# Kernel optimization log

Hardware: AMD Instinct MI355X
Metric: run time of the kernel (lower is better)

## Reference

```python
import jax, jax.numpy as jnp
import numpy as np

N_IN, C, T, E, N_OUT, F = 50000, 64, 8, 800000, 50000, 64


def setup_inputs() -> dict:
    key = jax.random.key(0)
    k0, k1, k2, k3, k4 = jax.random.split(key, 5)
    node_features = jax.random.normal(k0, (N_IN, C), dtype=jnp.float32)
    edge_features = jax.random.normal(k1, (T, E), dtype=jnp.float32)
    idx_out = jax.random.randint(k2, (E,), 0, N_OUT)
    idx_in = jax.random.randint(k3, (E,), 0, N_IN)
    indices = jnp.stack([idx_out, idx_in], axis=1).astype(jnp.int64)  # [E, 2]
    # glorot-ish scale for kernel [T, C, F]
    scale = np.sqrt(2.0 / (C + F)).astype(np.float32)
    kernel = jax.random.normal(k4, (T, C, F), dtype=jnp.float32) * scale
    bias = jnp.zeros((F,), dtype=jnp.float32)
    return {
        "node_features": node_features,
        "edge_features": edge_features,
        "indices": indices,
        "kernel": kernel,
        "bias": bias,
        "out_size": N_OUT,
    }


def reference(node_features, edge_features, indices, kernel, bias, out_size):
    # sparse_conv (combine='unstack'):
    #   out[i] = sum_t ( segment_sum_{e: out(e)=i} ef[t,e] * x[in(e)] ) @ kernel[t] + bias
    gathered = node_features[indices[:, 1]]          # [E, C] irregular gather
    seg_ids = indices[:, 0]
    n_terms = kernel.shape[0]                        # small fixed structural dim
    out = jnp.zeros((out_size, kernel.shape[2]), dtype=node_features.dtype)
    for t in range(n_terms):
        weighted = edge_features[t][:, None] * gathered            # [E, C]
        agg = jax.ops.segment_sum(weighted, seg_ids, num_segments=out_size)  # [No, C]
        out = out + agg @ kernel[t]                                # [No, F]
    return out + bias
```

## Files before the change

kernel.cpp:

```cpp
#include <hip/hip_runtime.h>

constexpr int N_IN  = 50000;
constexpr int C     = 64;
constexpr int T     = 8;
constexpr int E     = 800000;
constexpr int N_OUT = 50000;
constexpr int F     = 64;

constexpr int CHUNK  = 2048;
constexpr int NCHUNK = (E + CHUNK - 1) / CHUNK;
constexpr int NBIN_S = (N_OUT + 255) / 256;
constexpr int CAP    = 5120;
static_assert(CAP < 8192, "rel index must fit 13 bits in the u32 pack");

constexpr size_t OFF_NFBF  = 0;
constexpr size_t OFF_KT    = 6400000;
constexpr size_t OFF_BCUR  = OFF_KT + 65536;
constexpr size_t OFF_START = OFF_BCUR + 1024;
constexpr size_t OFF_ENT   = OFF_START + 200064;
constexpr size_t OFF_ENT2  = OFF_ENT + 4014080;
constexpr size_t OFF_BINW  = OFF_ENT2 + 3200000;
static_assert(OFF_BINW % 16 == 0 && OFF_ENT % 16 == 0, "alignment");
static_assert((size_t)NBIN_S * CAP * 4 <= 4014080, "ent fits");

typedef __attribute__((ext_vector_type(8))) short short8;
typedef __attribute__((ext_vector_type(4))) float f32x4;

__device__ inline unsigned short f2bf(float x) {
    unsigned int u = __float_as_uint(x);
    unsigned int r = (u + 0x7FFFu + ((u >> 16) & 1u)) >> 16;
    return (unsigned short)r;
}
__device__ inline float bf2f(unsigned short u) {
    return __uint_as_float(((unsigned int)u) << 16);
}

constexpr int BS_BLOCKS = NCHUNK;
constexpr int NF_BLOCKS = (N_IN * C / 4 + 511) / 512;
constexpr int KT_BLOCKS = T * C * F / 512;

__global__ __launch_bounds__(512) void fused_prep_kernel(
        const float* __restrict__ nf,
        const float* __restrict__ Kmat,
        const float* __restrict__ ef,
        const int* __restrict__ idx,
        unsigned short* __restrict__ nf_bf,
        unsigned short* __restrict__ K_T,
        int* __restrict__ bincur,
        unsigned* __restrict__ ent,
        float* __restrict__ binw) {
    __shared__ int2 se[CHUNK];
    __shared__ int hist[NBIN_S];
    __shared__ int cur[NBIN_S];

    const int b   = blockIdx.x;
    const int tid = threadIdx.x;

    if (b < BS_BLOCKS) {
        for (int i = tid; i < NBIN_S; i += 512) hist[i] = 0;
        __syncthreads();
        const int e0 = b * CHUNK;
        const int n  = min(CHUNK, E - e0);
        for (int i = tid; i < n; i += 512) {
            int2 oi = ((const int2*)idx)[e0 + i];
            se[i] = oi;
            atomicAdd(&hist[oi.x >> 8], 1);
        }
        __syncthreads();
        for (int bb = tid; bb < NBIN_S; bb += 512) {
            int c = hist[bb];
            if (c > 0) cur[bb] = bb * CAP + atomicAdd(&bincur[bb], c);
        }
        __syncthreads();
        for (int i = tid; i < n; i += 512) {
            int2 oi = se[i];
            int bin = oi.x >> 8;
            int loc = oi.x & 255;
            float w[8];
#pragma unroll
            for (int t = 0; t < T; ++t) w[t] = ef[(size_t)t * E + e0 + i];
            int pos = atomicAdd(&cur[bin], 1);
            ent[pos] = ((unsigned)loc << 16) | (unsigned)oi.y;
            float4* dst = (float4*)(binw + (size_t)pos * 8);
            dst[0] = make_float4(w[0], w[1], w[2], w[3]);
            dst[1] = make_float4(w[4], w[5], w[6], w[7]);
        }
    } else if (b < BS_BLOCKS + NF_BLOCKS) {
        int i = (b - BS_BLOCKS) * 512 + tid;
        if (i < N_IN * C / 4) {
            float4 v = ((const float4*)nf)[i];
            unsigned int u0 = (unsigned int)f2bf(v.x) | ((unsigned int)f2bf(v.y) << 16);
            unsigned int u1 = (unsigned int)f2bf(v.z) | ((unsigned int)f2bf(v.w) << 16);
            ((uint2*)nf_bf)[i] = make_uint2(u0, u1);
        }
    } else {
        int k = (b - BS_BLOCKS - NF_BLOCKS) * 512 + tid;
        int f = k & 63;
        int c = (k >> 6) & 63;
        int t = k >> 12;
        K_T[f * 512 + t * 64 + c] = f2bf(Kmat[k]);
    }
}

__global__ __launch_bounds__(512) void permfix_kernel(const int* __restrict__ bincur,
                                                      const unsigned* __restrict__ ent,
                                                      int* __restrict__ start_g,
                                                      unsigned* __restrict__ ent2) {
    __shared__ int sh[768];
    const int tid = threadIdx.x;
    const int b   = blockIdx.x;

    sh[tid] = (tid < b) ? bincur[tid] : 0;
    __syncthreads();
#pragma unroll
    for (int off = 256; off >= 1; off >>= 1) {
        if (tid < off) sh[tid] += sh[tid + off];
        __syncthreads();
    }
    const int base2 = sh[0];
    const int cnt   = bincur[b];
    const int W0p   = b * CAP;
    __syncthreads();

    int* hist = sh;
    int* sc   = sh + 256;
    int* cur  = sh + 512;

    if (tid < 256) hist[tid] = 0;
    __syncthreads();
    for (int i = W0p + tid; i < W0p + cnt; i += 512)
        atomicAdd(&hist[ent[i] >> 16], 1);
    __syncthreads();

    if (tid < 256) sc[tid] = hist[tid];
    __syncthreads();
    for (int off = 1; off < 256; off <<= 1) {
        int x = 0;
        if (tid < 256 && tid >= off) x = sc[tid - off];
        __syncthreads();
        if (tid < 256 && tid >= off) sc[tid] += x;
        __syncthreads();
    }
    if (tid < 256) {
        int s = base2 + sc[tid] - hist[tid];
        int g = b * 256 + tid;
        if (g < N_OUT) start_g[g] = s;
        cur[tid] = s;
    }
    if (b == NBIN_S - 1 && tid == 0) start_g[N_OUT] = E;
    __syncthreads();

    for (int i = W0p + tid; i < W0p + cnt; i += 512) {
        unsigned u = ent[i];
        int loc = (int)(u >> 16);
        int pos = atomicAdd(&cur[loc], 1);
        ent2[pos] = ((unsigned)(i - W0p) << 16) | (u & 0xFFFFu);
    }
}

__global__ __launch_bounds__(256) void aggregate_kernel(const unsigned short* __restrict__ nf_bf,
                                                        const unsigned short* __restrict__ K_T,
                                                        const int* __restrict__ start,
                                                        const unsigned* __restrict__ ent2,
                                                        const float* __restrict__ binw,
                                                        const float* __restrict__ bias,
                                                        float* __restrict__ out) {
    __shared__ unsigned short A_lds[16][520];

    constexpr int NWG = N_OUT / 16;
    constexpr int Q = NWG / 8, R = NWG % 8;
    const int xc = blockIdx.x & 7;
    const int sl = blockIdx.x >> 3;
    const int orig = (xc < R ? xc * (Q + 1) : R * (Q + 1) + (xc - R) * Q) + sl;

    const int wave = threadIdx.x >> 6;
    const int lane = threadIdx.x & 63;
    const int node_base = orig * 16;
    const int Wbase = (orig >> 4) * CAP;

    for (int q = 0; q < 4; ++q) {
        const int m = wave * 4 + q;
        const int o = node_base + m;
        const int s0 = __builtin_amdgcn_readfirstlane(start[o]);
        const int s1 = __builtin_amdgcn_readfirstlane(start[o + 1]);

        float acc[8] = {0.f, 0.f, 0.f, 0.f, 0.f, 0.f, 0.f, 0.f};

        for (int base = s0; base < s1; base += 64) {
            const int cnt = min(64, s1 - base);
            int vv = (base + lane < s1) ? (int)ent2[base + lane] : 0;

            int j = 0;
            for (; j + 4 <= cnt; j += 4) {
                const int v0 = __builtin_amdgcn_readlane(vv, j + 0);
                const int v1 = __builtin_amdgcn_readlane(vv, j + 1);
                const int v2 = __builtin_amdgcn_readlane(vv, j + 2);
                const int v3 = __builtin_amdgcn_readlane(vv, j + 3);
                float x0 = bf2f(nf_bf[(size_t)(v0 & 0xFFFF) * 64 + lane]);
                float x1 = bf2f(nf_bf[(size_t)(v1 & 0xFFFF) * 64 + lane]);
                float x2 = bf2f(nf_bf[(size_t)(v2 & 0xFFFF) * 64 + lane]);
                float x3 = bf2f(nf_bf[(size_t)(v3 & 0xFFFF) * 64 + lane]);
                const float* w0 = binw + (size_t)(Wbase + (((unsigned)v0) >> 16)) * 8;
                const float* w1 = binw + (size_t)(Wbase + (((unsigned)v1) >> 16)) * 8;
                const float* w2 = binw + (size_t)(Wbase + (((unsigned)v2) >> 16)) * 8;
                const float* w3 = binw + (size_t)(Wbase + (((unsigned)v3) >> 16)) * 8;
#pragma unroll
                for (int t = 0; t < T; ++t) {
                    acc[t] += w0[t] * x0;
                    acc[t] += w1[t] * x1;
                    acc[t] += w2[t] * x2;
                    acc[t] += w3[t] * x3;
                }
            }
            for (; j < cnt; ++j) {
                const int v0 = __builtin_amdgcn_readlane(vv, j);
                float x0 = bf2f(nf_bf[(size_t)(v0 & 0xFFFF) * 64 + lane]);
                const float* w0 = binw + (size_t)(Wbase + (((unsigned)v0) >> 16)) * 8;
#pragma unroll
                for (int t = 0; t < T; ++t) acc[t] += w0[t] * x0;
            }
        }

#pragma unroll
        for (int t = 0; t < T; ++t) A_lds[m][t * 64 + lane] = f2bf(acc[t]);
    }
    __syncthreads();

    const int mrow = lane & 15;
    const int kb   = lane >> 4;
    const int fcol = wave * 16 + mrow;

    f32x4 acc4 = {0.f, 0.f, 0.f, 0.f};
#pragma unroll
    for (int s = 0; s < 16; ++s) {
        const int k0 = s * 32 + kb * 8;
        short8 a = *(const short8*)&A_lds[mrow][k0];
        short8 b = *(const short8*)(K_T + (size_t)fcol * 512 + k0);
        acc4 = __builtin_amdgcn_mfma_f32_16x16x32_bf16(a, b, acc4, 0, 0, 0);
    }

    const float bv = bias[fcol];
#pragma unroll
    for (int r = 0; r < 4; ++r) {
        const int m = kb * 4 + r;
        out[(size_t)(node_base + m) * F + fcol] = acc4[r] + bv;
    }
}

extern "C" void kernel_launch(void* const* d_in, const int* in_sizes, int n_in,
                              void* d_out, int out_size, void* d_ws, size_t ws_size,
                              hipStream_t stream) {
    const float* nf   = (const float*)d_in[0];
    const float* ef   = (const float*)d_in[1];
    const int*   idx  = (const int*)d_in[2];
    const float* Kmat = (const float*)d_in[3];
    const float* bias = (const float*)d_in[4];
    float*       out  = (float*)d_out;

    char* ws = (char*)d_ws;
    unsigned short* nf_bf  = (unsigned short*)(ws + OFF_NFBF);
    unsigned short* K_T    = (unsigned short*)(ws + OFF_KT);
    int*            bincur = (int*)(ws + OFF_BCUR);
    int*            start  = (int*)(ws + OFF_START);
    unsigned*       ent    = (unsigned*)(ws + OFF_ENT);
    unsigned*       ent2   = (unsigned*)(ws + OFF_ENT2);
    float*          binw   = (float*)(ws + OFF_BINW);

    hipMemsetAsync(bincur, 0, NBIN_S * sizeof(int), stream);
    fused_prep_kernel<<<BS_BLOCKS + NF_BLOCKS + KT_BLOCKS, 512, 0, stream>>>(
        nf, Kmat, ef, idx, nf_bf, K_T, bincur, ent, binw);
    permfix_kernel<<<NBIN_S, 512, 0, stream>>>(bincur, ent, start, ent2);
    aggregate_kernel<<<N_OUT / 16, 256, 0, stream>>>(
        nf_bf, K_T, start, ent2, binw, bias, out);
}
```

Baseline: 185.0 us.

## Fuse per-bin sort into aggregation kernel with 64-node bins

Shrinks output bins to 64 nodes and removes the separate permutation/start kernel: each aggregation block now counting-sorts its bin's entries in LDS and then gathers, aggregates and applies the MFMA projection for its 64 nodes. This removes a kernel launch and the global round trip of the sorted entry and start arrays. In exchange, far fewer, larger blocks run, a serial sort phase precedes compute in each block, and entries past the fixed per-bin capacity are silently dropped. The chunk size also changes and indices are reread instead of staged in LDS.

```diff
diff --git a/kernel.cpp b/kernel.cpp
--- a/kernel.cpp
+++ b/kernel.cpp
@@ -7,21 +7,19 @@
 constexpr int N_OUT = 50000;
 constexpr int F     = 64;
 
-constexpr int CHUNK  = 2048;
+constexpr int BINN   = 64;
+constexpr int NBIN   = (N_OUT + BINN - 1) / BINN;
+constexpr int CAP    = 1344;
+constexpr int CHUNK  = 4096;
 constexpr int NCHUNK = (E + CHUNK - 1) / CHUNK;
-constexpr int NBIN_S = (N_OUT + 255) / 256;
-constexpr int CAP    = 5120;
-static_assert(CAP < 8192, "rel index must fit 13 bits in the u32 pack");
-
-constexpr size_t OFF_NFBF  = 0;
-constexpr size_t OFF_KT    = 6400000;
-constexpr size_t OFF_BCUR  = OFF_KT + 65536;
-constexpr size_t OFF_START = OFF_BCUR + 1024;
-constexpr size_t OFF_ENT   = OFF_START + 200064;
-constexpr size_t OFF_ENT2  = OFF_ENT + 4014080;
-constexpr size_t OFF_BINW  = OFF_ENT2 + 3200000;
-static_assert(OFF_BINW % 16 == 0 && OFF_ENT % 16 == 0, "alignment");
-static_assert((size_t)NBIN_S * CAP * 4 <= 4014080, "ent fits");
+
+constexpr size_t OFF_NFBF = 0;
+constexpr size_t OFF_KT   = 6400000;
+constexpr size_t OFF_BCUR = OFF_KT + 65536;
+constexpr size_t OFF_ENT  = OFF_BCUR + 3200;
+constexpr size_t OFF_BINW = OFF_ENT + 4204032;
+static_assert(OFF_ENT % 16 == 0 && OFF_BINW % 16 == 0, "alignment");
+static_assert((size_t)NBIN * CAP * 4 == 4204032, "ent size");
 
 typedef __attribute__((ext_vector_type(8))) short short8;
 typedef __attribute__((ext_vector_type(4))) float f32x4;
@@ -49,41 +47,38 @@
         int* __restrict__ bincur,
         unsigned* __restrict__ ent,
         float* __restrict__ binw) {
-    __shared__ int2 se[CHUNK];
-    __shared__ int hist[NBIN_S];
-    __shared__ int cur[NBIN_S];
+    __shared__ int hist[NBIN];
+    __shared__ int cur[NBIN];
 
     const int b   = blockIdx.x;
     const int tid = threadIdx.x;
 
     if (b < BS_BLOCKS) {
-        for (int i = tid; i < NBIN_S; i += 512) hist[i] = 0;
+        for (int i = tid; i < NBIN; i += 512) hist[i] = 0;
         __syncthreads();
         const int e0 = b * CHUNK;
         const int n  = min(CHUNK, E - e0);
+        for (int i = tid; i < n; i += 512)
+            atomicAdd(&hist[((const int2*)idx)[e0 + i].x >> 6], 1);
+        __syncthreads();
+        for (int bb = tid; bb < NBIN; bb += 512) {
+            int c = hist[bb];
+            if (c > 0) cur[bb] = bb * CAP + atomicAdd(&bincur[bb], c);
+        }
+        __syncthreads();
         for (int i = tid; i < n; i += 512) {
             int2 oi = ((const int2*)idx)[e0 + i];
-            se[i] = oi;
-            atomicAdd(&hist[oi.x >> 8], 1);
-        }
-        __syncthreads();
-        for (int bb = tid; bb < NBIN_S; bb += 512) {
-            int c = hist[bb];
-            if (c > 0) cur[bb] = bb * CAP + atomicAdd(&bincur[bb], c);
-        }
-        __syncthreads();
-        for (int i = tid; i < n; i += 512) {
-            int2 oi = se[i];
-            int bin = oi.x >> 8;
-            int loc = oi.x & 255;
+            int bin = oi.x >> 6;
             float w[8];
 #pragma unroll
             for (int t = 0; t < T; ++t) w[t] = ef[(size_t)t * E + e0 + i];
             int pos = atomicAdd(&cur[bin], 1);
-            ent[pos] = ((unsigned)loc << 16) | (unsigned)oi.y;
-            float4* dst = (float4*)(binw + (size_t)pos * 8);
-            dst[0] = make_float4(w[0], w[1], w[2], w[3]);
-            dst[1] = make_float4(w[4], w[5], w[6], w[7]);
+            if (pos < (bin + 1) * CAP) {
+                ent[pos] = ((unsigned)(oi.x & 63) << 16) | (unsigned)oi.y;
+                float4* dst = (float4*)(binw + (size_t)pos * 8);
+                dst[0] = make_float4(w[0], w[1], w[2], w[3]);
+                dst[1] = make_float4(w[4], w[5], w[6], w[7]);
+            }
         }
     } else if (b < BS_BLOCKS + NF_BLOCKS) {
         int i = (b - BS_BLOCKS) * 512 + tid;
@@ -102,108 +97,86 @@
     }
 }
 
-__global__ __launch_bounds__(512) void permfix_kernel(const int* __restrict__ bincur,
-                                                      const unsigned* __restrict__ ent,
-                                                      int* __restrict__ start_g,
-                                                      unsigned* __restrict__ ent2) {
-    __shared__ int sh[768];
-    const int tid = threadIdx.x;
-    const int b   = blockIdx.x;
-
-    sh[tid] = (tid < b) ? bincur[tid] : 0;
-    __syncthreads();
-#pragma unroll
-    for (int off = 256; off >= 1; off >>= 1) {
-        if (tid < off) sh[tid] += sh[tid + off];
-        __syncthreads();
-    }
-    const int base2 = sh[0];
-    const int cnt   = bincur[b];
-    const int W0p   = b * CAP;
-    __syncthreads();
-
-    int* hist = sh;
-    int* sc   = sh + 256;
-    int* cur  = sh + 512;
-
-    if (tid < 256) hist[tid] = 0;
-    __syncthreads();
-    for (int i = W0p + tid; i < W0p + cnt; i += 512)
-        atomicAdd(&hist[ent[i] >> 16], 1);
-    __syncthreads();
-
-    if (tid < 256) sc[tid] = hist[tid];
-    __syncthreads();
-    for (int off = 1; off < 256; off <<= 1) {
+__global__ __launch_bounds__(512) void aggbin_kernel(
+        const unsigned short* __restrict__ nf_bf,
+        const unsigned short* __restrict__ K_T,
+        const int* __restrict__ bincur,
+        const unsigned* __restrict__ ent,
+        const float* __restrict__ binw,
+        const float* __restrict__ bias,
+        float* __restrict__ out) {
+    __shared__ unsigned sent[CAP];
+    __shared__ unsigned short A_lds[32][520];
+    __shared__ int hist[BINN];
+    __shared__ int sstart[BINN + 1];
+    __shared__ int cur[BINN];
+
+    const int b    = blockIdx.x;
+    const int tid  = threadIdx.x;
+    const int wave = tid >> 6;
+    const int lane = tid & 63;
+    const int W0p  = b * CAP;
+    const int cnt  = min(bincur[b], CAP);
+
+    if (tid < BINN) hist[tid] = 0;
+    __syncthreads();
+    for (int i = tid; i < cnt; i += 512)
+        atomicAdd(&hist[ent[W0p + i] >> 16], 1);
+    __syncthreads();
+    if (tid < BINN) sstart[tid] = hist[tid];
+    __syncthreads();
+    for (int off = 1; off < BINN; off <<= 1) {
         int x = 0;
-        if (tid < 256 && tid >= off) x = sc[tid - off];
-        __syncthreads();
-        if (tid < 256 && tid >= off) sc[tid] += x;
-        __syncthreads();
-    }
-    if (tid < 256) {
-        int s = base2 + sc[tid] - hist[tid];
-        int g = b * 256 + tid;
-        if (g < N_OUT) start_g[g] = s;
-        cur[tid] = s;
-    }
-    if (b == NBIN_S - 1 && tid == 0) start_g[N_OUT] = E;
-    __syncthreads();
-
-    for (int i = W0p + tid; i < W0p + cnt; i += 512) {
-        unsigned u = ent[i];
-        int loc = (int)(u >> 16);
-        int pos = atomicAdd(&cur[loc], 1);
-        ent2[pos] = ((unsigned)(i - W0p) << 16) | (u & 0xFFFFu);
-    }
-}
-
-__global__ __launch_bounds__(256) void aggregate_kernel(const unsigned short* __restrict__ nf_bf,
-                                                        const unsigned short* __restrict__ K_T,
-                                                        const int* __restrict__ start,
-                                                        const unsigned* __restrict__ ent2,
-                                                        const float* __restrict__ binw,
-                                                        const float* __restrict__ bias,
-                                                        float* __restrict__ out) {
-    __shared__ unsigned short A_lds[16][520];
-
-    constexpr int NWG = N_OUT / 16;
-    constexpr int Q = NWG / 8, R = NWG % 8;
-    const int xc = blockIdx.x & 7;
-    const int sl = blockIdx.x >> 3;
-    const int orig = (xc < R ? xc * (Q + 1) : R * (Q + 1) + (xc - R) * Q) + sl;
-
-    const int wave = threadIdx.x >> 6;
-    const int lane = threadIdx.x & 63;
-    const int node_base = orig * 16;
-    const int Wbase = (orig >> 4) * CAP;
-
-    for (int q = 0; q < 4; ++q) {
-        const int m = wave * 4 + q;
-        const int o = node_base + m;
-        const int s0 = __builtin_amdgcn_readfirstlane(start[o]);
-        const int s1 = __builtin_amdgcn_readfirstlane(start[o + 1]);
-
-        float acc[8] = {0.f, 0.f, 0.f, 0.f, 0.f, 0.f, 0.f, 0.f};
-
-        for (int base = s0; base < s1; base += 64) {
-            const int cnt = min(64, s1 - base);
-            int vv = (base + lane < s1) ? (int)ent2[base + lane] : 0;
-
-            int j = 0;
-            for (; j + 4 <= cnt; j += 4) {
-                const int v0 = __builtin_amdgcn_readlane(vv, j + 0);
-                const int v1 = __builtin_amdgcn_readlane(vv, j + 1);
-                const int v2 = __builtin_amdgcn_readlane(vv, j + 2);
-                const int v3 = __builtin_amdgcn_readlane(vv, j + 3);
-                float x0 = bf2f(nf_bf[(size_t)(v0 & 0xFFFF) * 64 + lane]);
-                float x1 = bf2f(nf_bf[(size_t)(v1 & 0xFFFF) * 64 + lane]);
-                float x2 = bf2f(nf_bf[(size_t)(v2 & 0xFFFF) * 64 + lane]);
-                float x3 = bf2f(nf_bf[(size_t)(v3 & 0xFFFF) * 64 + lane]);
-                const float* w0 = binw + (size_t)(Wbase + (((unsigned)v0) >> 16)) * 8;
-                const float* w1 = binw + (size_t)(Wbase + (((unsigned)v1) >> 16)) * 8;
-                const float* w2 = binw + (size_t)(Wbase + (((unsigned)v2) >> 16)) * 8;
-                const float* w3 = binw + (size_t)(Wbase + (((unsigned)v3) >> 16)) * 8;
+        if (tid < BINN && tid >= off) x = sstart[tid - off];
+        __syncthreads();
+        if (tid < BINN && tid >= off) sstart[tid] += x;
+        __syncthreads();
+    }
+    int excl = 0;
+    if (tid < BINN) excl = sstart[tid] - hist[tid];
+    __syncthreads();
+    if (tid < BINN) { sstart[tid] = excl; cur[tid] = excl; }
+    if (tid == 0) sstart[BINN] = cnt;
+    __syncthreads();
+    for (int i = tid; i < cnt; i += 512) {
+        unsigned u = ent[W0p + i];
+        int pos = atomicAdd(&cur[u >> 16], 1);
+        sent[pos] = ((unsigned)i << 16) | (u & 0xFFFFu);
+    }
+    __syncthreads();
+
+    const int mrow  = lane & 15;
+    const int kb    = lane >> 4;
+    const int fcol  = (wave & 3) * 16 + mrow;
+    const int rbase = (wave >> 2) * 16;
+    const float bv  = bias[fcol];
+
+    for (int g = 0; g < 2; ++g) {
+        for (int q = 0; q < 4; ++q) {
+            const int nl = g * 32 + wave * 4 + q;
+            const int s0 = sstart[nl];
+            const int s1 = sstart[nl + 1];
+
+            float acc[8] = {0.f, 0.f, 0.f, 0.f, 0.f, 0.f, 0.f, 0.f};
+
+            int j = s0;
+            for (; j + 4 <= s1; j += 4) {
+                const unsigned e0 = sent[j + 0];
+                const unsigned e1 = sent[j + 1];
+                const unsigned e2 = sent[j + 2];
+                const unsigned e3 = sent[j + 3];
+                float x0 = bf2f(nf_bf[(size_t)(e0 & 0xFFFFu) * 64 + lane]);
+                float x1 = bf2f(nf_bf[(size_t)(e1 & 0xFFFFu) * 64 + lane]);
+                float x2 = bf2f(nf_bf[(size_t)(e2 & 0xFFFFu) * 64 + lane]);
+                float x3 = bf2f(nf_bf[(size_t)(e3 & 0xFFFFu) * 64 + lane]);
+                const float* w0 = binw + ((size_t)W0p +
+                    (unsigned)__builtin_amdgcn_readfirstlane((int)(e0 >> 16))) * 8;
+                const float* w1 = binw + ((size_t)W0p +
+                    (unsigned)__builtin_amdgcn_readfirstlane((int)(e1 >> 16))) * 8;
+                const float* w2 = binw + ((size_t)W0p +
+                    (unsigned)__builtin_amdgcn_readfirstlane((int)(e2 >> 16))) * 8;
+                const float* w3 = binw + ((size_t)W0p +
+                    (unsigned)__builtin_amdgcn_readfirstlane((int)(e3 >> 16))) * 8;
 #pragma unroll
                 for (int t = 0; t < T; ++t) {
                     acc[t] += w0[t] * x0;
@@ -212,38 +185,36 @@
                     acc[t] += w3[t] * x3;
                 }
             }
-            for (; j < cnt; ++j) {
-                const int v0 = __builtin_amdgcn_readlane(vv, j);
-                float x0 = bf2f(nf_bf[(size_t)(v0 & 0xFFFF) * 64 + lane]);
-                const float* w0 = binw + (size_t)(Wbase + (((unsigned)v0) >> 16)) * 8;
+            for (; j < s1; ++j) {
+                const unsigned e0 = sent[j];
+                float x0 = bf2f(nf_bf[(size_t)(e0 & 0xFFFFu) * 64 + lane]);
+                const float* w0 = binw + ((size_t)W0p +
+                    (unsigned)__builtin_amdgcn_readfirstlane((int)(e0 >> 16))) * 8;
 #pragma unroll
                 for (int t = 0; t < T; ++t) acc[t] += w0[t] * x0;
             }
-        }
-
-#pragma unroll
-        for (int t = 0; t < T; ++t) A_lds[m][t * 64 + lane] = f2bf(acc[t]);
-    }
-    __syncthreads();
-
-    const int mrow = lane & 15;
-    const int kb   = lane >> 4;
-    const int fcol = wave * 16 + mrow;
-
-    f32x4 acc4 = {0.f, 0.f, 0.f, 0.f};
-#pragma unroll
-    for (int s = 0; s < 16; ++s) {
-        const int k0 = s * 32 + kb * 8;
-        short8 a = *(const short8*)&A_lds[mrow][k0];
-        short8 b = *(const short8*)(K_T + (size_t)fcol * 512 + k0);
-        acc4 = __builtin_amdgcn_mfma_f32_16x16x32_bf16(a, b, acc4, 0, 0, 0);
-    }
-
-    const float bv = bias[fcol];
-#pragma unroll
-    for (int r = 0; r < 4; ++r) {
-        const int m = kb * 4 + r;
-        out[(size_t)(node_base + m) * F + fcol] = acc4[r] + bv;
+
+#pragma unroll
+            for (int t = 0; t < T; ++t)
+                A_lds[wave * 4 + q][t * 64 + lane] = f2bf(acc[t]);
+        }
+        __syncthreads();
+
+        f32x4 acc4 = {0.f, 0.f, 0.f, 0.f};
+#pragma unroll
+        for (int s = 0; s < 16; ++s) {
+            const int k0 = s * 32 + kb * 8;
+            short8 a = *(const short8*)&A_lds[rbase + mrow][k0];
+            short8 bm = *(const short8*)(K_T + (size_t)fcol * 512 + k0);
+            acc4 = __builtin_amdgcn_mfma_f32_16x16x32_bf16(a, bm, acc4, 0, 0, 0);
+        }
+#pragma unroll
+        for (int r = 0; r < 4; ++r) {
+            const int orow = b * BINN + g * 32 + rbase + kb * 4 + r;
+            if (orow < N_OUT)
+                out[(size_t)orow * F + fcol] = acc4[r] + bv;
+        }
+        __syncthreads();
     }
 }
 
@@ -261,15 +232,12 @@
     unsigned short* nf_bf  = (unsigned short*)(ws + OFF_NFBF);
     unsigned short* K_T    = (unsigned short*)(ws + OFF_KT);
     int*            bincur = (int*)(ws + OFF_BCUR);
-    int*            start  = (int*)(ws + OFF_START);
     unsigned*       ent    = (unsigned*)(ws + OFF_ENT);
-    unsigned*       ent2   = (unsigned*)(ws + OFF_ENT2);
     float*          binw   = (float*)(ws + OFF_BINW);
 
-    hipMemsetAsync(bincur, 0, NBIN_S * sizeof(int), stream);
+    hipMemsetAsync(bincur, 0, NBIN * sizeof(int), stream);
     fused_prep_kernel<<<BS_BLOCKS + NF_BLOCKS + KT_BLOCKS, 512, 0, stream>>>(
         nf, Kmat, ef, idx, nf_bf, K_T, bincur, ent, binw);
-    permfix_kernel<<<NBIN_S, 512, 0, stream>>>(bincur, ent, start, ent2);
-    aggregate_kernel<<<N_OUT / 16, 256, 0, stream>>>(
-        nf_bf, K_T, start, ent2, binw, bias, out);
-}
+    aggbin_kernel<<<NBIN, 512, 0, stream>>>(
+        nf_bf, K_T, bincur, ent, binw, bias, out);
+}
```

Result: slower. 196.2 us (+6.1%).

## Sort chunk edges by bin in shared memory before scattering to global bins

Applied to the files above, without the earlier changes.

The binning pass now does a local counting sort within each chunk: a histogram, a block-wide prefix scan, and a shared-memory scatter, then a second pass writes entries so that consecutive threads hit consecutive global positions within each bin. This turns the old random per-edge atomic placement into coalesced contiguous writes of ent and binw. The edge-feature reads become gathered through the sorted offset, which may reduce their coalescing. It also adds CAP overflow guards and clamps the count in permfix, at the cost of an extra scan and more shared memory.

```diff
diff --git a/kernel.cpp b/kernel.cpp
--- a/kernel.cpp
+++ b/kernel.cpp
@@ -11,7 +11,6 @@
 constexpr int NCHUNK = (E + CHUNK - 1) / CHUNK;
 constexpr int NBIN_S = (N_OUT + 255) / 256;
 constexpr int CAP    = 5120;
-static_assert(CAP < 8192, "rel index must fit 13 bits in the u32 pack");
 
 constexpr size_t OFF_NFBF  = 0;
 constexpr size_t OFF_KT    = 6400000;
@@ -20,8 +19,7 @@
 constexpr size_t OFF_ENT   = OFF_START + 200064;
 constexpr size_t OFF_ENT2  = OFF_ENT + 4014080;
 constexpr size_t OFF_BINW  = OFF_ENT2 + 3200000;
-static_assert(OFF_BINW % 16 == 0 && OFF_ENT % 16 == 0, "alignment");
-static_assert((size_t)NBIN_S * CAP * 4 <= 4014080, "ent fits");
+static_assert(OFF_ENT % 16 == 0 && OFF_BINW % 16 == 0, "alignment");
 
 typedef __attribute__((ext_vector_type(8))) short short8;
 typedef __attribute__((ext_vector_type(4))) float f32x4;
@@ -49,9 +47,14 @@
         int* __restrict__ bincur,
         unsigned* __restrict__ ent,
         float* __restrict__ binw) {
-    __shared__ int2 se[CHUNK];
     __shared__ int hist[NBIN_S];
+    __shared__ int scb[NBIN_S];
     __shared__ int cur[NBIN_S];
+    __shared__ int gdel[NBIN_S];
+    __shared__ int sscan[256];
+    __shared__ unsigned sgu[CHUNK];
+    __shared__ unsigned short sge[CHUNK];
+    __shared__ unsigned char sgb[CHUNK];
 
     const int b   = blockIdx.x;
     const int tid = threadIdx.x;
@@ -61,29 +64,52 @@
         __syncthreads();
         const int e0 = b * CHUNK;
         const int n  = min(CHUNK, E - e0);
+        for (int i = tid; i < n; i += 512)
+            atomicAdd(&hist[((const int2*)idx)[e0 + i].x >> 8], 1);
+        __syncthreads();
+        if (tid < 256) sscan[tid] = (tid < NBIN_S) ? hist[tid] : 0;
+        __syncthreads();
+        for (int off = 1; off < 256; off <<= 1) {
+            int x = 0;
+            if (tid < 256 && tid >= off) x = sscan[tid - off];
+            __syncthreads();
+            if (tid < 256 && tid >= off) sscan[tid] += x;
+            __syncthreads();
+        }
+        if (tid < NBIN_S) {
+            int e = sscan[tid] - hist[tid];
+            scb[tid] = e;
+            cur[tid] = e;
+        }
+        __syncthreads();
+        for (int bb = tid; bb < NBIN_S; bb += 512) {
+            int c = hist[bb];
+            if (c > 0)
+                gdel[bb] = bb * CAP + atomicAdd(&bincur[bb], c) - scb[bb];
+        }
+        __syncthreads();
         for (int i = tid; i < n; i += 512) {
             int2 oi = ((const int2*)idx)[e0 + i];
-            se[i] = oi;
-            atomicAdd(&hist[oi.x >> 8], 1);
-        }
-        __syncthreads();
-        for (int bb = tid; bb < NBIN_S; bb += 512) {
-            int c = hist[bb];
-            if (c > 0) cur[bb] = bb * CAP + atomicAdd(&bincur[bb], c);
+            int bin = oi.x >> 8;
+            int r = atomicAdd(&cur[bin], 1);
+            sgu[r] = ((unsigned)(oi.x & 255) << 16) | (unsigned)oi.y;
+            sge[r] = (unsigned short)i;
+            sgb[r] = (unsigned char)bin;
         }
         __syncthreads();
         for (int i = tid; i < n; i += 512) {
-            int2 oi = se[i];
-            int bin = oi.x >> 8;
-            int loc = oi.x & 255;
-            float w[8];
-#pragma unroll
-            for (int t = 0; t < T; ++t) w[t] = ef[(size_t)t * E + e0 + i];
-            int pos = atomicAdd(&cur[bin], 1);
-            ent[pos] = ((unsigned)loc << 16) | (unsigned)oi.y;
-            float4* dst = (float4*)(binw + (size_t)pos * 8);
-            dst[0] = make_float4(w[0], w[1], w[2], w[3]);
-            dst[1] = make_float4(w[4], w[5], w[6], w[7]);
+            int bin  = sgb[i];
+            int pos  = gdel[bin] + i;
+            if (pos < (bin + 1) * CAP) {
+                int eoff = sge[i];
+                float w[8];
+#pragma unroll
+                for (int t = 0; t < T; ++t) w[t] = ef[(size_t)t * E + e0 + eoff];
+                ent[pos] = sgu[i];
+                float4* dst = (float4*)(binw + (size_t)pos * 8);
+                dst[0] = make_float4(w[0], w[1], w[2], w[3]);
+                dst[1] = make_float4(w[4], w[5], w[6], w[7]);
+            }
         }
     } else if (b < BS_BLOCKS + NF_BLOCKS) {
         int i = (b - BS_BLOCKS) * 512 + tid;
@@ -118,7 +144,7 @@
         __syncthreads();
     }
     const int base2 = sh[0];
-    const int cnt   = bincur[b];
+    const int cnt   = min(bincur[b], CAP);
     const int W0p   = b * CAP;
     __syncthreads();
 
```

Result: no change. 181.8 us (-1.7%).
